# Performance work log

Measured on AMD Instinct MI355X. Metric: run time of the kernel, lower is better.

Reference implementation:

```python
import jax, jax.numpy as jnp
import numpy as np

ALPHA = 0.2  # module hardcodes a = 0.2


def _triplet_total(outputs, labels):
    # Faithful vectorization of the nested-loop mining:
    #  - sort samples by label (stable, like python sorted with key=label)
    #  - anchor p1 = first element of each contiguous label group
    #  - positives p2 = remaining members of the group; ap = ||p1-p2||^2
    #  - negatives = every sample with a different label
    #  - per (p2, neg): add (ap - an + alpha) for an in {||p1-n||^2, ||p2-n||^2}
    #    iff ap < an and ap - an + alpha > 0  (i.e. 0 < an - ap < alpha)
    order = jnp.argsort(labels)          # stable sort, matches python sorted
    x = outputs[order]                   # [n, d]
    lab = labels[order]                  # [n]
    n = x.shape[0]
    idx = jnp.arange(n)
    is_start = jnp.concatenate([jnp.ones((1,), bool), lab[1:] != lab[:-1]])
    # index of the group-start (anchor) for every position
    anchor_of = jax.lax.cummax(jnp.where(is_start, idx, 0))

    # pairwise squared distances Dm[i,j] = ||x_i - x_j||^2
    sq = jnp.sum(x * x, axis=-1)                       # [n]
    Dm = sq[:, None] + sq[None, :] - 2.0 * (x @ x.T)   # [n, n]

    ap = Dm[anchor_of, idx]   # [n]   ||p1 - p2||^2 for each potential positive
    an1 = Dm[anchor_of, :]    # [n,n] ||p1 - neg||^2
    an2 = Dm                  # [n,n] ||p2 - neg||^2

    pos_mask = ~is_start                         # p2 ranges over non-anchor rows
    neg_mask = lab[:, None] != lab[None, :]      # negatives: different label
    valid = pos_mask[:, None] & neg_mask         # [n, n]

    def hinge(an):
        d = ap[:, None] - an
        return jnp.where((d < 0) & (d + ALPHA > 0), d + ALPHA, 0.0)

    contrib = jnp.where(valid, hinge(an1) + hinge(an2), 0.0)
    return jnp.sum(contrib)


def setup_inputs() -> dict:
    key = jax.random.key(0)
    k1, k2 = jax.random.split(key)
    N, D, C = 8192, 128, 512
    outputs = jax.random.normal(k1, (N, D), dtype=jnp.float32)
    labels = jax.random.randint(k2, (N,), 0, C, dtype=jnp.int32)
    return {"outputs": outputs, "labels": labels}


def reference(outputs, labels):
    return _triplet_total(outputs, labels)
```

## Files before the change

### kernel.cpp

```cpp
#include <hip/hip_runtime.h>
#include <limits.h>
#include <stdint.h>

#define ALPHA 0.2f
#define HALFA 0.1f
static constexpr int N = 8192;
static constexpr int D = 128;
static constexpr int C = 512;
static constexpr int BT = 128;
static constexpr int GR = D / 8;
static constexpr int SL = BT + 1;
static constexpr int MAXG = 64;
static constexpr int NB = N / BT;
static constexpr int NTRI = NB * (NB + 1) / 2;
static constexpr int T1 = (C / 64) * (N / BT);
static constexpr int NTILES = T1 + NTRI;
static constexpr int GRID = 512;

using half8    = __attribute__((ext_vector_type(8))) _Float16;
using floatx16 = __attribute__((ext_vector_type(16))) float;

__device__ __forceinline__ floatx16 zerov() { floatx16 v = {0.f}; return v; }

__device__ __forceinline__ half8 cvt8(float4 v0, float4 v1) {
    half8 h;
    h[0] = (_Float16)v0.x; h[1] = (_Float16)v0.y; h[2] = (_Float16)v0.z; h[3] = (_Float16)v0.w;
    h[4] = (_Float16)v1.x; h[5] = (_Float16)v1.y; h[6] = (_Float16)v1.z; h[7] = (_Float16)v1.w;
    return h;
}

__device__ __forceinline__ float ss8(float4 v0, float4 v1) {
    return v0.x*v0.x + v0.y*v0.y + v0.z*v0.z + v0.w*v0.w
         + v1.x*v1.x + v1.y*v1.y + v1.z*v1.z + v1.w*v1.w;
}


__launch_bounds__(256)
__global__ void k_prep(const float* __restrict__ x, const int* __restrict__ labels,
                       _Float16* __restrict__ xh, float* __restrict__ sq,
                       int* __restrict__ anchorg, float* __restrict__ ap,
                       float* __restrict__ out) {
    __shared__ int sAnc[C];
    const int tid = threadIdx.x;
    if (blockIdx.x == 0 && tid == 0) out[0] = 0.f;
    for (int i = tid; i < C; i += 256) sAnc[i] = INT_MAX;
    __syncthreads();
    const int4* lab4 = (const int4*)labels;
    for (int t = tid; t < N / 4; t += 256) {
        int4 lv = lab4[t];
        int base = 4 * t;
        atomicMin(&sAnc[lv.x], base);
        atomicMin(&sAnc[lv.y], base + 1);
        atomicMin(&sAnc[lv.z], base + 2);
        atomicMin(&sAnc[lv.w], base + 3);
    }
    __syncthreads();
    if (tid < 2) {
        int c = blockIdx.x * 2 + tid;
        int a = sAnc[c];
        anchorg[c] = (a == INT_MAX) ? -1 : a;
    }

    const int r = blockIdx.x * 32 + (tid >> 3);
    const int sub = tid & 7;
    const float4* src = (const float4*)(x + (size_t)r * D) + sub * 4;
    half8* dst = (half8*)(xh + (size_t)r * D) + sub * 2;
    half8 hj[2];
    float ssj = 0.f;
#pragma unroll
    for (int i = 0; i < 2; ++i) {
        float4 v0 = src[2 * i], v1 = src[2 * i + 1];
        hj[i] = cvt8(v0, v1);
        dst[i] = hj[i];
        ssj += ss8(v0, v1);
    }
    ssj += __shfl_xor(ssj, 1); ssj += __shfl_xor(ssj, 2); ssj += __shfl_xor(ssj, 4);

    const int a = sAnc[labels[r]];
    const float4* asrc = (const float4*)(x + (size_t)a * D) + sub * 4;
    float ssa = 0.f, dot = 0.f;
#pragma unroll
    for (int i = 0; i < 2; ++i) {
        float4 a0 = asrc[2 * i], a1 = asrc[2 * i + 1];
        half8 ha = cvt8(a0, a1);
        ssa += ss8(a0, a1);
#pragma unroll
        for (int e = 0; e < 8; ++e) dot = fmaf((float)ha[e], (float)hj[i][e], dot);
    }
    ssa += __shfl_xor(ssa, 1); ssa += __shfl_xor(ssa, 2); ssa += __shfl_xor(ssa, 4);
    dot += __shfl_xor(dot, 1); dot += __shfl_xor(dot, 2); dot += __shfl_xor(dot, 4);
    if (sub == 0) {
        sq[r] = ssj;
        ap[r] = ssa + ssj - 2.f * dot;
    }
}


__device__ __forceinline__ void dec_tri(int t, int& br, int& bc) {
    int rem = t, b = 0;
    while (rem >= NB - b) { rem -= NB - b; ++b; }
    br = b; bc = b + rem;
}

__launch_bounds__(512, 4)
__global__ void k_main(const _Float16* __restrict__ xh, const int* __restrict__ labels,
                       const int* __restrict__ anchor, const float* __restrict__ sq,
                       const float* __restrict__ ap, float* __restrict__ out) {
    __shared__ __align__(16) _Float16 BsH[GR * SL * 8];
    __shared__ __align__(16) float sge[64 * MAXG];
    __shared__ float4 rowE[BT];
    __shared__ float4 colE[BT];
    __shared__ int   sArow[64];
    __shared__ float sSqA[64];
    __shared__ int   sCnt[64];
    __shared__ float wsum[8];
    half8* Bs = (half8*)BsH;

    const int tid = threadIdx.x;
    const int lane = tid & 63, w = tid >> 6;
    const int m = lane & 31, q = lane >> 5;
    const int wr = w >> 1, wc = w & 1;
    const int wr2 = w >> 2, wc4 = w & 3;
    const int sg = tid & 15, sr0 = tid >> 4;
    float local = 0.f;

    half8 af[8];
    half8 breg[4];

    for (int s = blockIdx.x; s < NTILES; s += GRID) {
        int i0n = 0, j0n = 0;
        const bool hasNext = (s + GRID < NTILES);
        if (hasNext) {
            int brn, bcn; dec_tri(s + GRID - T1, brn, bcn);
            i0n = brn * BT; j0n = bcn * BT;
        }

        if (s < T1) {
            const int cb = s >> 6, jb = s & 63;
            const int c0 = cb * 64, j0 = jb * BT;

            if (tid < 64) {
                int a = anchor[c0 + tid];
                int ar = (a < 0) ? 0 : a;
                sArow[tid] = ar; sSqA[tid] = sq[ar]; sCnt[tid] = 0;
            } else if (tid < 192) {
                int j = j0 + tid - 64;
                colE[tid - 64] = make_float4(sq[j], __int_as_float(labels[j]), 0.f, 0.f);
            }
            {
                float4 big = make_float4(1e30f, 1e30f, 1e30f, 1e30f);
                ((float4*)sge)[tid * 2] = big; ((float4*)sge)[tid * 2 + 1] = big;
            }
            __syncthreads();

            {
                int arow = sArow[wr2 * 32 + m];
                const half8* aptr = (const half8*)(xh + (size_t)arow * D) + q;
#pragma unroll
                for (int k = 0; k < 8; ++k) af[k] = aptr[2 * k];
            }
#pragma unroll
            for (int i = 0; i < 4; ++i) {
                int row = sr0 + 32 * i;
                Bs[sg * SL + row] = *((const half8*)(xh + (size_t)(j0 + row) * D) + sg);
            }
            {
                const int4* lab4 = (const int4*)labels;
                for (int t = tid; t < N / 4; t += 512) {
                    int4 lv = lab4[t];
                    int base = 4 * t;
#pragma unroll
                    for (int kk = 0; kk < 4; ++kk) {
                        int l = (kk == 0) ? lv.x : (kk == 1) ? lv.y : (kk == 2) ? lv.z : lv.w;
                        int li = l - c0;
                        if ((unsigned)li < 64u) {
                            int idx = base + kk;
                            if (idx != sArow[li]) {
                                int slot = atomicAdd(&sCnt[li], 1);
                                if (slot < MAXG) sge[li * MAXG + slot] = ap[idx] + HALFA;
                            }
                        }
                    }
                }
            }
            __syncthreads();

            floatx16 acc = zerov();
#pragma unroll
            for (int k = 0; k < 8; ++k) {
                half8 b0 = Bs[(2 * k + q) * SL + wc4 * 32 + m];
                acc = __builtin_amdgcn_mfma_f32_32x32x16_f16(af[k], b0, acc, 0, 0, 0);
            }
            if (hasNext) {
                const half8* aptr = (const half8*)(xh + (size_t)(i0n + wr * 32 + m) * D) + q;
#pragma unroll
                for (int k = 0; k < 8; ++k) af[k] = aptr[2 * k];
            }
            {
                float4 cj = colE[wc4 * 32 + m];
                float sqj = cj.x; int labj = __float_as_int(cj.y);
#pragma unroll
                for (int rr = 0; rr < 16; ++rr) {
                    int row = wr2 * 32 + (rr & 3) + 8 * (rr >> 2) + 4 * q;
                    float Dv = fmaf(-2.f, acc[rr], sSqA[row] + sqj);
                    bool vld = (labj != c0 + row);
                    int n = sCnt[row]; n = (n > MAXG) ? MAXG : n;
                    int nf = (n + 3) & ~3;
                    for (int gb = 0; gb < nf; gb += 4) {
                        float4 ev = *(const float4*)&sge[row * MAXG + gb];
                        float u;
                        u = ev.x - Dv; if (vld && __builtin_fabsf(u) < HALFA) local += u + HALFA;
                        u = ev.y - Dv; if (vld && __builtin_fabsf(u) < HALFA) local += u + HALFA;
                        u = ev.z - Dv; if (vld && __builtin_fabsf(u) < HALFA) local += u + HALFA;
                        u = ev.w - Dv; if (vld && __builtin_fabsf(u) < HALFA) local += u + HALFA;
                    }
                }
            }
            if (hasNext) {
#pragma unroll
                for (int i = 0; i < 4; ++i)
                    breg[i] = *((const half8*)(xh + (size_t)(j0n + sr0 + 32 * i) * D) + sg);
            }
            __syncthreads();
        } else {
            int br, bc; dec_tri(s - T1, br, bc);
            const int i0 = br * BT, j0 = bc * BT;
            const bool diag = (br == bc);

            if (tid < BT) {
                int i = i0 + tid;
                int li = labels[i]; int a = anchor[li];
                float sqi = sq[i];
                float e2 = (i == a) ? -1e30f : ap[i] + HALFA - sqi;
                rowE[tid] = make_float4(e2, __int_as_float(li), sqi, 0.f);
            } else if (tid < 2 * BT) {
                int t = tid - BT;
                int j = j0 + t;
                int lj = labels[j]; int a = anchor[lj];
                float sqj = sq[j];
                float e2 = (j == a) ? -1e30f : ap[j] + HALFA - sqj;
                colE[t] = make_float4(e2, __int_as_float(lj), sqj, 0.f);
            }
#pragma unroll
            for (int i = 0; i < 4; ++i)
                Bs[sg * SL + sr0 + 32 * i] = breg[i];
            __syncthreads();

            floatx16 acc0 = zerov(), acc1 = zerov();
#pragma unroll
            for (int k = 0; k < 8; ++k) {
                half8 b0 = Bs[(2 * k + q) * SL + wc * 64 + m];
                half8 b1 = Bs[(2 * k + q) * SL + wc * 64 + 32 + m];
                acc0 = __builtin_amdgcn_mfma_f32_32x32x16_f16(af[k], b0, acc0, 0, 0, 0);
                acc1 = __builtin_amdgcn_mfma_f32_32x32x16_f16(af[k], b1, acc1, 0, 0, 0);
            }
            if (hasNext) {
                const half8* aptr = (const half8*)(xh + (size_t)(i0n + wr * 32 + m) * D) + q;
#pragma unroll
                for (int k = 0; k < 8; ++k) af[k] = aptr[2 * k];
            }

            float sqjv[2], e2j[2]; int labj[2];
            { float4 cj = colE[wc * 64 + m];      e2j[0] = cj.x; labj[0] = __float_as_int(cj.y); sqjv[0] = cj.z; }
            { float4 cj = colE[wc * 64 + 32 + m]; e2j[1] = cj.x; labj[1] = __float_as_int(cj.y); sqjv[1] = cj.z; }

#pragma unroll
            for (int rr = 0; rr < 16; ++rr) {
                int row = wr * 32 + (rr & 3) + 8 * (rr >> 2) + 4 * q;
                float4 re = rowE[row];
                float e2i = re.x, sqi = re.z;
                int labi = __float_as_int(re.y);
                {
                    float dot = acc0[rr];
                    if (labi != labj[0]) {
                        float u2 = fmaf(2.f, dot, e2i - sqjv[0]);
                        if (__builtin_fabsf(u2) < HALFA) local += u2 + HALFA;
                        if (!diag) {
                            float u2b = fmaf(2.f, dot, e2j[0] - sqi);
                            if (__builtin_fabsf(u2b) < HALFA) local += u2b + HALFA;
                        }
                    }
                }
                {
                    float dot = acc1[rr];
                    if (labi != labj[1]) {
                        float u2 = fmaf(2.f, dot, e2i - sqjv[1]);
                        if (__builtin_fabsf(u2) < HALFA) local += u2 + HALFA;
                        if (!diag) {
                            float u2b = fmaf(2.f, dot, e2j[1] - sqi);
                            if (__builtin_fabsf(u2b) < HALFA) local += u2b + HALFA;
                        }
                    }
                }
            }
            if (hasNext) {
#pragma unroll
                for (int i = 0; i < 4; ++i)
                    breg[i] = *((const half8*)(xh + (size_t)(j0n + sr0 + 32 * i) * D) + sg);
            }
            __syncthreads();
        }
    }

#pragma unroll
    for (int off = 32; off; off >>= 1) local += __shfl_down(local, off);
    if (lane == 0) wsum[w] = local;
    __syncthreads();
    if (tid == 0) {
        float ssum = 0.f;
#pragma unroll
        for (int i = 0; i < 8; ++i) ssum += wsum[i];
        atomicAdd(out, ssum);
    }
}


extern "C" void kernel_launch(void* const* d_in, const int* in_sizes, int n_in,
                              void* d_out, int out_size, void* d_ws, size_t ws_size,
                              hipStream_t stream) {
    const float* x = (const float*)d_in[0];
    const int* labels = (const int*)d_in[1];
    float* out = (float*)d_out;

    char* p = (char*)d_ws;
    int* anchor = (int*)p;        p += C * 4;
    float* sq = (float*)p;        p += N * 4;
    float* ap = (float*)p;        p += N * 4;
    p = (char*)(((uintptr_t)p + 255) & ~(uintptr_t)255);
    _Float16* xh = (_Float16*)p;

    k_prep<<<N / 32, 256, 0, stream>>>(x, labels, xh, sq, anchor, ap, out);
    k_main<<<GRID, 512, 0, stream>>>(xh, labels, anchor, sq, ap, out);
}
```

Baseline: 118.1 us.

## Replace grid-stride tile loop with dedicated blocks and paired-row triangle strips

The persistent grid-stride loop over mixed tile types is replaced by a fixed grid. One block handles each anchor tile, and 16 blocks share each pair of complementary triangle rows (k and 63-k, 65 tiles in total). Within a strip the A fragment and row metadata are reloaded only when the block row changes, and column metadata is double-buffered alongside the B prefetch. This aims to balance work, cut the serial triangle decode, and reuse A loads. In exchange the grid grows, the load-balancing of the grid-stride loop is lost, and the occupancy hint in launch_bounds drops from 4 to 2.

```diff
diff --git a/kernel.cpp b/kernel.cpp
--- a/kernel.cpp
+++ b/kernel.cpp
@@ -12,10 +12,10 @@
 static constexpr int SL = BT + 1;
 static constexpr int MAXG = 64;
 static constexpr int NB = N / BT;
-static constexpr int NTRI = NB * (NB + 1) / 2;
-static constexpr int T1 = (C / 64) * (N / BT);
-static constexpr int NTILES = T1 + NTRI;
-static constexpr int GRID = 512;
+static constexpr int NT1 = (C / 64) * (N / BT);
+static constexpr int NSP = NB / 2;
+static constexpr int SPB = 16;
+static constexpr int GRID = NT1 + NSP * SPB;
 
 using half8    = __attribute__((ext_vector_type(8))) _Float16;
 using floatx16 = __attribute__((ext_vector_type(16))) float;
@@ -32,6 +32,11 @@
 __device__ __forceinline__ float ss8(float4 v0, float4 v1) {
     return v0.x*v0.x + v0.y*v0.y + v0.z*v0.z + v0.w*v0.w
          + v1.x*v1.x + v1.y*v1.y + v1.z*v1.z + v1.w*v1.w;
+}
+
+__device__ __forceinline__ void dec_sp(int k, int t, int lenA, int& br, int& bc) {
+    if (t < lenA) { br = k;      bc = k + t; }
+    else          { br = 63 - k; bc = 63 - k + (t - lenA); }
 }
 
 
@@ -96,20 +101,14 @@
 }
 
 
-__device__ __forceinline__ void dec_tri(int t, int& br, int& bc) {
-    int rem = t, b = 0;
-    while (rem >= NB - b) { rem -= NB - b; ++b; }
-    br = b; bc = b + rem;
-}
-
-__launch_bounds__(512, 4)
+__launch_bounds__(512, 2)
 __global__ void k_main(const _Float16* __restrict__ xh, const int* __restrict__ labels,
                        const int* __restrict__ anchor, const float* __restrict__ sq,
                        const float* __restrict__ ap, float* __restrict__ out) {
     __shared__ __align__(16) _Float16 BsH[GR * SL * 8];
     __shared__ __align__(16) float sge[64 * MAXG];
     __shared__ float4 rowE[BT];
-    __shared__ float4 colE[BT];
+    __shared__ float4 colE[2][BT];
     __shared__ int   sArow[64];
     __shared__ float sSqA[64];
     __shared__ int   sCnt[64];
@@ -119,150 +118,161 @@
     const int tid = threadIdx.x;
     const int lane = tid & 63, w = tid >> 6;
     const int m = lane & 31, q = lane >> 5;
-    const int wr = w >> 1, wc = w & 1;
-    const int wr2 = w >> 2, wc4 = w & 3;
     const int sg = tid & 15, sr0 = tid >> 4;
     float local = 0.f;
 
-    half8 af[8];
-    half8 breg[4];
-
-    for (int s = blockIdx.x; s < NTILES; s += GRID) {
-        int i0n = 0, j0n = 0;
-        const bool hasNext = (s + GRID < NTILES);
-        if (hasNext) {
-            int brn, bcn; dec_tri(s + GRID - T1, brn, bcn);
-            i0n = brn * BT; j0n = bcn * BT;
-        }
-
-        if (s < T1) {
-            const int cb = s >> 6, jb = s & 63;
-            const int c0 = cb * 64, j0 = jb * BT;
-
-            if (tid < 64) {
-                int a = anchor[c0 + tid];
-                int ar = (a < 0) ? 0 : a;
-                sArow[tid] = ar; sSqA[tid] = sq[ar]; sCnt[tid] = 0;
-            } else if (tid < 192) {
-                int j = j0 + tid - 64;
-                colE[tid - 64] = make_float4(sq[j], __int_as_float(labels[j]), 0.f, 0.f);
-            }
-            {
-                float4 big = make_float4(1e30f, 1e30f, 1e30f, 1e30f);
-                ((float4*)sge)[tid * 2] = big; ((float4*)sge)[tid * 2 + 1] = big;
-            }
-            __syncthreads();
-
-            {
-                int arow = sArow[wr2 * 32 + m];
-                const half8* aptr = (const half8*)(xh + (size_t)arow * D) + q;
-#pragma unroll
-                for (int k = 0; k < 8; ++k) af[k] = aptr[2 * k];
-            }
-#pragma unroll
-            for (int i = 0; i < 4; ++i) {
-                int row = sr0 + 32 * i;
-                Bs[sg * SL + row] = *((const half8*)(xh + (size_t)(j0 + row) * D) + sg);
-            }
-            {
-                const int4* lab4 = (const int4*)labels;
-                for (int t = tid; t < N / 4; t += 512) {
-                    int4 lv = lab4[t];
-                    int base = 4 * t;
-#pragma unroll
-                    for (int kk = 0; kk < 4; ++kk) {
-                        int l = (kk == 0) ? lv.x : (kk == 1) ? lv.y : (kk == 2) ? lv.z : lv.w;
-                        int li = l - c0;
-                        if ((unsigned)li < 64u) {
-                            int idx = base + kk;
-                            if (idx != sArow[li]) {
-                                int slot = atomicAdd(&sCnt[li], 1);
-                                if (slot < MAXG) sge[li * MAXG + slot] = ap[idx] + HALFA;
-                            }
+    if ((int)blockIdx.x < NT1) {
+        const int cb = blockIdx.x >> 6, jb = blockIdx.x & 63;
+        const int c0 = cb * 64, j0 = jb * BT;
+        const int wr2 = w >> 2, wc4 = w & 3;
+
+        if (tid < 64) {
+            int a = anchor[c0 + tid];
+            int ar = (a < 0) ? 0 : a;
+            sArow[tid] = ar; sSqA[tid] = sq[ar]; sCnt[tid] = 0;
+        } else if (tid < 192) {
+            int j = j0 + tid - 64;
+            colE[0][tid - 64] = make_float4(sq[j], __int_as_float(labels[j]), 0.f, 0.f);
+        }
+        {
+            float4 big = make_float4(1e30f, 1e30f, 1e30f, 1e30f);
+            ((float4*)sge)[tid * 2] = big; ((float4*)sge)[tid * 2 + 1] = big;
+        }
+        __syncthreads();
+
+        half8 af[8];
+        {
+            int arow = sArow[wr2 * 32 + m];
+            const half8* aptr = (const half8*)(xh + (size_t)arow * D) + q;
+#pragma unroll
+            for (int k = 0; k < 8; ++k) af[k] = aptr[2 * k];
+        }
+#pragma unroll
+        for (int i = 0; i < 4; ++i) {
+            int row = sr0 + 32 * i;
+            Bs[sg * SL + row] = *((const half8*)(xh + (size_t)(j0 + row) * D) + sg);
+        }
+        {
+            const int4* lab4 = (const int4*)labels;
+            for (int t = tid; t < N / 4; t += 512) {
+                int4 lv = lab4[t];
+                int base = 4 * t;
+#pragma unroll
+                for (int kk = 0; kk < 4; ++kk) {
+                    int l = (kk == 0) ? lv.x : (kk == 1) ? lv.y : (kk == 2) ? lv.z : lv.w;
+                    int li = l - c0;
+                    if ((unsigned)li < 64u) {
+                        int idx = base + kk;
+                        if (idx != sArow[li]) {
+                            int slot = atomicAdd(&sCnt[li], 1);
+                            if (slot < MAXG) sge[li * MAXG + slot] = ap[idx] + HALFA;
                         }
                     }
                 }
             }
-            __syncthreads();
-
-            floatx16 acc = zerov();
-#pragma unroll
-            for (int k = 0; k < 8; ++k) {
-                half8 b0 = Bs[(2 * k + q) * SL + wc4 * 32 + m];
-                acc = __builtin_amdgcn_mfma_f32_32x32x16_f16(af[k], b0, acc, 0, 0, 0);
-            }
-            if (hasNext) {
-                const half8* aptr = (const half8*)(xh + (size_t)(i0n + wr * 32 + m) * D) + q;
-#pragma unroll
-                for (int k = 0; k < 8; ++k) af[k] = aptr[2 * k];
-            }
-            {
-                float4 cj = colE[wc4 * 32 + m];
-                float sqj = cj.x; int labj = __float_as_int(cj.y);
-#pragma unroll
-                for (int rr = 0; rr < 16; ++rr) {
-                    int row = wr2 * 32 + (rr & 3) + 8 * (rr >> 2) + 4 * q;
-                    float Dv = fmaf(-2.f, acc[rr], sSqA[row] + sqj);
-                    bool vld = (labj != c0 + row);
-                    int n = sCnt[row]; n = (n > MAXG) ? MAXG : n;
-                    int nf = (n + 3) & ~3;
-                    for (int gb = 0; gb < nf; gb += 4) {
-                        float4 ev = *(const float4*)&sge[row * MAXG + gb];
-                        float u;
-                        u = ev.x - Dv; if (vld && __builtin_fabsf(u) < HALFA) local += u + HALFA;
-                        u = ev.y - Dv; if (vld && __builtin_fabsf(u) < HALFA) local += u + HALFA;
-                        u = ev.z - Dv; if (vld && __builtin_fabsf(u) < HALFA) local += u + HALFA;
-                        u = ev.w - Dv; if (vld && __builtin_fabsf(u) < HALFA) local += u + HALFA;
-                    }
-                }
-            }
-            if (hasNext) {
-#pragma unroll
-                for (int i = 0; i < 4; ++i)
-                    breg[i] = *((const half8*)(xh + (size_t)(j0n + sr0 + 32 * i) * D) + sg);
-            }
-            __syncthreads();
-        } else {
-            int br, bc; dec_tri(s - T1, br, bc);
-            const int i0 = br * BT, j0 = bc * BT;
-            const bool diag = (br == bc);
-
+        }
+        __syncthreads();
+
+        floatx16 acc = zerov();
+#pragma unroll
+        for (int k = 0; k < 8; ++k) {
+            half8 b0 = Bs[(2 * k + q) * SL + wc4 * 32 + m];
+            acc = __builtin_amdgcn_mfma_f32_32x32x16_f16(af[k], b0, acc, 0, 0, 0);
+        }
+
+        float4 cj = colE[0][wc4 * 32 + m];
+        float sqj = cj.x; int labj = __float_as_int(cj.y);
+#pragma unroll
+        for (int rr = 0; rr < 16; ++rr) {
+            int row = wr2 * 32 + (rr & 3) + 8 * (rr >> 2) + 4 * q;
+            float Dv = fmaf(-2.f, acc[rr], sSqA[row] + sqj);
+            bool vld = (labj != c0 + row);
+            int n = sCnt[row]; n = (n > MAXG) ? MAXG : n;
+            int nf = (n + 3) & ~3;
+            for (int gb = 0; gb < nf; gb += 4) {
+                float4 ev = *(const float4*)&sge[row * MAXG + gb];
+                float u;
+                u = ev.x - Dv; if (vld && __builtin_fabsf(u) < HALFA) local += u + HALFA;
+                u = ev.y - Dv; if (vld && __builtin_fabsf(u) < HALFA) local += u + HALFA;
+                u = ev.z - Dv; if (vld && __builtin_fabsf(u) < HALFA) local += u + HALFA;
+                u = ev.w - Dv; if (vld && __builtin_fabsf(u) < HALFA) local += u + HALFA;
+            }
+        }
+    } else {
+        const int bi = blockIdx.x - NT1;
+        const int k = bi >> 4, p = bi & 15;
+        const int lenA = 64 - k;
+        const int wr = w >> 1, wc = w & 1;
+        int cbuf = 0, cur_br = -1;
+        half8 af[8], breg[4];
+
+        {
+            int br0, bc0; dec_sp(k, p, lenA, br0, bc0);
+            int j0 = bc0 * BT;
+#pragma unroll
+            for (int i = 0; i < 4; ++i)
+                breg[i] = *((const half8*)(xh + (size_t)(j0 + sr0 + 32 * i) * D) + sg);
             if (tid < BT) {
-                int i = i0 + tid;
-                int li = labels[i]; int a = anchor[li];
-                float sqi = sq[i];
-                float e2 = (i == a) ? -1e30f : ap[i] + HALFA - sqi;
-                rowE[tid] = make_float4(e2, __int_as_float(li), sqi, 0.f);
-            } else if (tid < 2 * BT) {
-                int t = tid - BT;
-                int j = j0 + t;
+                int j = j0 + tid;
                 int lj = labels[j]; int a = anchor[lj];
                 float sqj = sq[j];
                 float e2 = (j == a) ? -1e30f : ap[j] + HALFA - sqj;
-                colE[t] = make_float4(e2, __int_as_float(lj), sqj, 0.f);
-            }
+                colE[0][tid] = make_float4(e2, __int_as_float(lj), sqj, 0.f);
+            }
+        }
+
+        for (int t = p; t < 65; t += SPB) {
+            int br, bc; dec_sp(k, t, lenA, br, bc);
+            const int i0 = br * BT, j0n_unused = bc;
+            (void)j0n_unused;
+            const bool diag = (br == bc);
+
+            if (br != cur_br) {
+                cur_br = br;
+                const half8* aptr = (const half8*)(xh + (size_t)(i0 + wr * 32 + m) * D) + q;
+#pragma unroll
+                for (int kk = 0; kk < 8; ++kk) af[kk] = aptr[2 * kk];
+                if (tid < BT) {
+                    int i = i0 + tid;
+                    int li = labels[i]; int a = anchor[li];
+                    float sqi = sq[i];
+                    float e2 = (i == a) ? -1e30f : ap[i] + HALFA - sqi;
+                    rowE[tid] = make_float4(e2, __int_as_float(li), sqi, 0.f);
+                }
+            }
+
 #pragma unroll
             for (int i = 0; i < 4; ++i)
                 Bs[sg * SL + sr0 + 32 * i] = breg[i];
             __syncthreads();
 
+            if (t + SPB < 65) {
+                int brn, bcn; dec_sp(k, t + SPB, lenA, brn, bcn);
+                int j0n = bcn * BT;
+#pragma unroll
+                for (int i = 0; i < 4; ++i)
+                    breg[i] = *((const half8*)(xh + (size_t)(j0n + sr0 + 32 * i) * D) + sg);
+                if (tid < BT) {
+                    int j = j0n + tid;
+                    int lj = labels[j]; int a = anchor[lj];
+                    float sqj = sq[j];
+                    float e2 = (j == a) ? -1e30f : ap[j] + HALFA - sqj;
+                    colE[cbuf ^ 1][tid] = make_float4(e2, __int_as_float(lj), sqj, 0.f);
+                }
+            }
+
             floatx16 acc0 = zerov(), acc1 = zerov();
 #pragma unroll
-            for (int k = 0; k < 8; ++k) {
-                half8 b0 = Bs[(2 * k + q) * SL + wc * 64 + m];
-                half8 b1 = Bs[(2 * k + q) * SL + wc * 64 + 32 + m];
-                acc0 = __builtin_amdgcn_mfma_f32_32x32x16_f16(af[k], b0, acc0, 0, 0, 0);
-                acc1 = __builtin_amdgcn_mfma_f32_32x32x16_f16(af[k], b1, acc1, 0, 0, 0);
-            }
-            if (hasNext) {
-                const half8* aptr = (const half8*)(xh + (size_t)(i0n + wr * 32 + m) * D) + q;
-#pragma unroll
-                for (int k = 0; k < 8; ++k) af[k] = aptr[2 * k];
+            for (int kk = 0; kk < 8; ++kk) {
+                half8 b0 = Bs[(2 * kk + q) * SL + wc * 64 + m];
+                half8 b1 = Bs[(2 * kk + q) * SL + wc * 64 + 32 + m];
+                acc0 = __builtin_amdgcn_mfma_f32_32x32x16_f16(af[kk], b0, acc0, 0, 0, 0);
+                acc1 = __builtin_amdgcn_mfma_f32_32x32x16_f16(af[kk], b1, acc1, 0, 0, 0);
             }
 
             float sqjv[2], e2j[2]; int labj[2];
-            { float4 cj = colE[wc * 64 + m];      e2j[0] = cj.x; labj[0] = __float_as_int(cj.y); sqjv[0] = cj.z; }
-            { float4 cj = colE[wc * 64 + 32 + m]; e2j[1] = cj.x; labj[1] = __float_as_int(cj.y); sqjv[1] = cj.z; }
+            { float4 cj = colE[cbuf][wc * 64 + m];      e2j[0] = cj.x; labj[0] = __float_as_int(cj.y); sqjv[0] = cj.z; }
+            { float4 cj = colE[cbuf][wc * 64 + 32 + m]; e2j[1] = cj.x; labj[1] = __float_as_int(cj.y); sqjv[1] = cj.z; }
 
 #pragma unroll
             for (int rr = 0; rr < 16; ++rr) {
@@ -293,11 +303,7 @@
                     }
                 }
             }
-            if (hasNext) {
-#pragma unroll
-                for (int i = 0; i < 4; ++i)
-                    breg[i] = *((const half8*)(xh + (size_t)(j0n + sr0 + 32 * i) * D) + sg);
-            }
+            cbuf ^= 1;
             __syncthreads();
         }
     }
@@ -307,10 +313,10 @@
     if (lane == 0) wsum[w] = local;
     __syncthreads();
     if (tid == 0) {
-        float ssum = 0.f;
-#pragma unroll
-        for (int i = 0; i < 8; ++i) ssum += wsum[i];
-        atomicAdd(out, ssum);
+        float s = 0.f;
+#pragma unroll
+        for (int i = 0; i < 8; ++i) s += wsum[i];
+        atomicAdd(out, s);
     }
 }
 
```

After: 113.4 us. 1.04x faster.
